# Kernel tuning notes

Hardware: AMD Instinct MI355X
Metric: run time of the kernel (lower is better)

Reference implementation:

```python
import jax, jax.numpy as jnp
import numpy as np

B, T, N, FI, FO = 4, 8, 1024, 64, 64
ALPHA = 0.2          # LeakyReLU negative slope
NEG_INF = -1e12      # matches torch's -1000000000000.0


def setup_inputs() -> dict:
    key = jax.random.key(0)
    k0, k1, k2, k3, k4 = jax.random.split(key, 5)
    inp = jax.random.normal(k0, (B, T, N, FI), dtype=jnp.float32)
    u = jax.random.uniform(k1, (T, N, N), dtype=jnp.float32)
    adj = jnp.where(u > 0.9, u, 0.0)
    # att_mask: [batch, node, seq] in {0,1}
    att_mask = (jax.random.uniform(k2, (B, N, T)) > 0.2).astype(jnp.float32)
    # xavier-ish init (gain 1.414)
    W = jax.random.normal(k3, (FI, FO), dtype=jnp.float32) * (1.414 * np.sqrt(2.0 / (FI + FO)))
    a = jax.random.normal(k4, (2 * FO, 1), dtype=jnp.float32) * (1.414 * np.sqrt(2.0 / (2 * FO + 1)))
    return {"adj": adj, "inp": inp, "att_mask": att_mask, "W": W, "a": a}


def reference(adj, inp, att_mask, W, a):
    Fo = W.shape[1]
    h = jnp.einsum('btnf,fo->btno', inp, W)               # [B,T,N,Fo]
    # additive decomposition of a^T [h_i || h_j] = a1.h_i + a2.h_j
    a1 = a[:Fo, 0]
    a2 = a[Fo:, 0]
    s1 = jnp.einsum('btno,o->btn', h, a1)                 # contributes along rows (i)
    s2 = jnp.einsum('btno,o->btn', h, a2)                 # contributes along cols (j)
    e = s1[..., :, None] + s2[..., None, :]               # [B,T,N,N]
    e = jnp.where(e > 0, e, ALPHA * e)                    # LeakyReLU
    att = jnp.where(adj > 0, e * adj, NEG_INF)            # adj broadcasts over batch
    att = jax.nn.softmax(att, axis=-1)
    m = jnp.transpose(att_mask, (0, 2, 1))                # [B,T,N]
    att = att * (m[..., :, None] * m[..., None, :])       # outer-product mask
    # dropout is identity in eval mode
    h_prime = jnp.einsum('btij,btjo->btio', att, h)       # [B,T,N,Fo]
    return jax.nn.elu(h_prime)                            # concat=True path
```

## Files before the change

### kernel.cpp

```cpp
#include <hip/hip_runtime.h>
#include <hip/hip_bf16.h>
#include <math.h>

#define N_NODES 1024
#define T_DIM 8

typedef __bf16 bf16x8 __attribute__((ext_vector_type(8)));
typedef float  f32x4  __attribute__((ext_vector_type(4)));

__device__ __forceinline__ float readlane_f(float v, int l) {
    return __uint_as_float(__builtin_amdgcn_readlane(__float_as_uint(v), l));
}

__global__ __launch_bounds__(256) void gat_h_kernel(
    const float* __restrict__ inp, const float* __restrict__ W,
    const float* __restrict__ a,
    __bf16* __restrict__ hT, float* __restrict__ s1w, float* __restrict__ s2w)
{
    __shared__ float Wl[64 * 64];
    __shared__ float xl[64 * 64];
    __shared__ __bf16 htl[64 * 66];

    const int tid  = threadIdx.x;
    const int blk  = blockIdx.x;
    const int bt   = blk >> 4;
    const int n0   = (blk & 15) * 64;
    const int lane = tid & 63;
    const int wave = tid >> 6;

    const float4* W4  = (const float4*)W;
    float4*       Wl4 = (float4*)Wl;
    const float4* x4  = (const float4*)(inp + (size_t)(bt * N_NODES + n0) * 64);
    float4*       xl4 = (float4*)xl;
#pragma unroll
    for (int k = 0; k < 4; ++k) {
        Wl4[tid + k * 256] = W4[tid + k * 256];
        xl4[tid + k * 256] = x4[tid + k * 256];
    }
    const float a1 = a[lane];
    const float a2 = a[64 + lane];
    __syncthreads();

#pragma unroll 1
    for (int rg = 0; rg < 16; rg += 4) {
        float xr[4], acc[4];
#pragma unroll
        for (int q = 0; q < 4; ++q) {
            xr[q]  = xl[(wave * 16 + rg + q) * 64 + lane];
            acc[q] = 0.f;
        }
#pragma unroll
        for (int f = 0; f < 64; ++f) {
            float w = Wl[f * 64 + lane];
#pragma unroll
            for (int q = 0; q < 4; ++q)
                acc[q] = fmaf(readlane_f(xr[q], f), w, acc[q]);
        }
#pragma unroll
        for (int q = 0; q < 4; ++q) {
            const int r = wave * 16 + rg + q;
            float v1 = acc[q] * a1, v2 = acc[q] * a2;
#pragma unroll
            for (int off = 32; off; off >>= 1) {
                v1 += __shfl_xor(v1, off, 64);
                v2 += __shfl_xor(v2, off, 64);
            }
            if (lane == 0) {
                s1w[bt * N_NODES + n0 + r] = v1;
                s2w[bt * N_NODES + n0 + r] = v2;
            }
            htl[lane * 66 + r] = (__bf16)acc[q];
        }
    }
    __syncthreads();

    {
        const int o  = tid >> 2;
        const int r0 = (tid & 3) * 16;
        unsigned u[8];
#pragma unroll
        for (int k = 0; k < 8; ++k)
            u[k] = *(const unsigned*)&htl[o * 66 + r0 + 2 * k];
        uint4* dst = (uint4*)(hT + (size_t)(bt * 64 + o) * N_NODES + n0 + r0);
        dst[0] = make_uint4(u[0], u[1], u[2], u[3]);
        dst[1] = make_uint4(u[4], u[5], u[6], u[7]);
    }
}

__global__ __launch_bounds__(64) void gat_attn_kernel(
    const float* __restrict__ adj, const float* __restrict__ att_mask,
    const __bf16* __restrict__ hT, const float* __restrict__ s1w,
    const float* __restrict__ s2w, float* __restrict__ out)
{
    __shared__ __align__(16) __bf16 p_l[16 * 72];

    const int bt    = blockIdx.y;
    const int b     = bt >> 3;
    const int t     = bt & 7;
    const int irow0 = blockIdx.x * 16;
    const int lane  = threadIdx.x;

    f32x4 acc[4];
#pragma unroll
    for (int nc = 0; nc < 4; ++nc) acc[nc] = (f32x4){0.f, 0.f, 0.f, 0.f};
    float lsum[16], s1v[16];
#pragma unroll
    for (int r = 0; r < 16; ++r) {
        lsum[r] = 0.f;
        s1v[r]  = s1w[bt * N_NODES + irow0 + r];
    }

    const float*  adjrow = adj + (size_t)t * N_NODES * N_NODES
                               + (size_t)irow0 * N_NODES + lane;
    const __bf16* hlane  = hT + (size_t)bt * 64 * N_NODES
                              + (size_t)(lane & 15) * N_NODES + (lane >> 4) * 8;
    const float*  s2bt   = s2w + bt * N_NODES;
    const float*  mbase  = att_mask + (size_t)b * N_NODES * T_DIM + t;
    __bf16* pwr = p_l + lane;
    const __bf16* prd = p_l + (lane & 15) * 72 + (lane >> 4) * 8;

    float  adjc[16];
    bf16x8 hc[8];
    float  s2c, mjc;
#pragma unroll
    for (int r = 0; r < 16; ++r) adjc[r] = adjrow[(size_t)r * N_NODES];
#pragma unroll
    for (int kc = 0; kc < 2; ++kc)
#pragma unroll
        for (int nc = 0; nc < 4; ++nc)
            hc[kc * 4 + nc] = *(const bf16x8*)(hlane + (size_t)nc * 16 * N_NODES + kc * 32);
    s2c = s2bt[lane];
    mjc = mbase[(size_t)lane * T_DIM];

#pragma unroll 2
    for (int it = 0; it < 16; ++it) {
        const int jn = (it < 15) ? (it + 1) * 64 : 0;

        float  adjn[16];
        bf16x8 hn[8];
#pragma unroll
        for (int r = 0; r < 16; ++r) adjn[r] = adjrow[(size_t)r * N_NODES + jn];
#pragma unroll
        for (int kc = 0; kc < 2; ++kc)
#pragma unroll
            for (int nc = 0; nc < 4; ++nc)
                hn[kc * 4 + nc] = *(const bf16x8*)(hlane + (size_t)nc * 16 * N_NODES + jn + kc * 32);
        const float s2n = s2bt[jn + lane];
        const float mjn = mbase[(size_t)(jn + lane) * T_DIM];

#pragma unroll
        for (int r = 0; r < 16; ++r) {
            float e = s1v[r] + s2c;
            e = (e > 0.f) ? e : 0.2f * e;
            float p = (adjc[r] > 0.f) ? __expf(e * adjc[r]) : 0.f;
            lsum[r] += p;
            pwr[r * 72] = (__bf16)(p * mjc);
        }

        bf16x8 af0 = *(const bf16x8*)(prd);
        bf16x8 af1 = *(const bf16x8*)(prd + 32);
#pragma unroll
        for (int nc = 0; nc < 4; ++nc)
            acc[nc] = __builtin_amdgcn_mfma_f32_16x16x32_bf16(af0, hc[nc], acc[nc], 0, 0, 0);
#pragma unroll
        for (int nc = 0; nc < 4; ++nc)
            acc[nc] = __builtin_amdgcn_mfma_f32_16x16x32_bf16(af1, hc[4 + nc], acc[nc], 0, 0, 0);

#pragma unroll
        for (int r = 0; r < 16; ++r) adjc[r] = adjn[r];
#pragma unroll
        for (int k = 0; k < 8; ++k) hc[k] = hn[k];
        s2c = s2n;
        mjc = mjn;
    }

#pragma unroll
    for (int r = 0; r < 16; ++r) {
#pragma unroll
        for (int off = 32; off; off >>= 1)
            lsum[r] += __shfl_xor(lsum[r], off, 64);
    }
    const int q = lane >> 4;
#pragma unroll
    for (int reg = 0; reg < 4; ++reg) {
        float ls = (q == 0) ? lsum[reg] : (q == 1) ? lsum[4 + reg]
                 : (q == 2) ? lsum[8 + reg] : lsum[12 + reg];
        const int i = irow0 + q * 4 + reg;
        float mi    = att_mask[((size_t)b * N_NODES + i) * T_DIM + t];
        float scale = mi / ls;
#pragma unroll
        for (int nc = 0; nc < 4; ++nc) {
            float v = acc[nc][reg] * scale;
            v = (v > 0.f) ? v : (__expf(v) - 1.f);
            out[((size_t)bt * N_NODES + i) * 64 + nc * 16 + (lane & 15)] = v;
        }
    }
}

extern "C" void kernel_launch(void* const* d_in, const int* in_sizes, int n_in,
                              void* d_out, int out_size, void* d_ws, size_t ws_size,
                              hipStream_t stream) {
    (void)in_sizes; (void)n_in; (void)out_size; (void)ws_size;
    const float* adj      = (const float*)d_in[0];
    const float* inp      = (const float*)d_in[1];
    const float* att_mask = (const float*)d_in[2];
    const float* W        = (const float*)d_in[3];
    const float* a        = (const float*)d_in[4];
    float* out = (float*)d_out;

    __bf16* hT  = (__bf16*)d_ws;
    float*  s1w = (float*)((char*)d_ws + (size_t)4 * 1024 * 1024);
    float*  s2w = s1w + 32 * N_NODES;

    gat_h_kernel<<<512, 256, 0, stream>>>(inp, W, a, hT, s1w, s2w);
    dim3 grid(64, 32);
    gat_attn_kernel<<<grid, 64, 0, stream>>>(adj, att_mask, hT, s1w, s2w, out);
}
```

Before: 140.6 us.

## Split attention key dimension across four waves with LDS reduction

The attention kernel now runs 256 threads per block, and each of four waves handles a quarter of the 1024 columns (j) for the same 16 rows. Each wave's partial MFMA accumulators and softmax row sums are written to shared memory and summed after a barrier before normalisation and ELU. The aim is more parallelism and latency hiding: 4x more waves over the same 2048 blocks, each with a shorter serial loop. The cost is extra LDS traffic, a block-wide sync, and a higher per-block LDS footprint.

Result: slower. 147.4 us (+4.8%).

```diff
diff --git a/kernel.cpp b/kernel.cpp
--- a/kernel.cpp
+++ b/kernel.cpp
@@ -87,18 +87,23 @@
     }
 }
 
-__global__ __launch_bounds__(64) void gat_attn_kernel(
+__global__ __launch_bounds__(256) void gat_attn_kernel(
     const float* __restrict__ adj, const float* __restrict__ att_mask,
     const __bf16* __restrict__ hT, const float* __restrict__ s1w,
     const float* __restrict__ s2w, float* __restrict__ out)
 {
-    __shared__ __align__(16) __bf16 p_l[16 * 72];
+    __shared__ __align__(16) __bf16 p_l[4][16 * 72];
+    __shared__ float accbuf[4][16][68];
+    __shared__ float lsumbuf[4][16];
 
     const int bt    = blockIdx.y;
     const int b     = bt >> 3;
     const int t     = bt & 7;
     const int irow0 = blockIdx.x * 16;
-    const int lane  = threadIdx.x;
+    const int tid   = threadIdx.x;
+    const int lane  = tid & 63;
+    const int wave  = tid >> 6;
+    const int j0    = wave * 256;
 
     f32x4 acc[4];
 #pragma unroll
@@ -111,13 +116,14 @@
     }
 
     const float*  adjrow = adj + (size_t)t * N_NODES * N_NODES
-                               + (size_t)irow0 * N_NODES + lane;
+                               + (size_t)irow0 * N_NODES + j0 + lane;
     const __bf16* hlane  = hT + (size_t)bt * 64 * N_NODES
-                              + (size_t)(lane & 15) * N_NODES + (lane >> 4) * 8;
-    const float*  s2bt   = s2w + bt * N_NODES;
-    const float*  mbase  = att_mask + (size_t)b * N_NODES * T_DIM + t;
-    __bf16* pwr = p_l + lane;
-    const __bf16* prd = p_l + (lane & 15) * 72 + (lane >> 4) * 8;
+                              + (size_t)(lane & 15) * N_NODES + j0 + (lane >> 4) * 8;
+    const float*  s2p    = s2w + bt * N_NODES + j0;
+    const float*  mp     = att_mask + (size_t)b * N_NODES * T_DIM + t
+                              + (size_t)j0 * T_DIM;
+    __bf16* pwr = p_l[wave] + lane;
+    const __bf16* prd = p_l[wave] + (lane & 15) * 72 + (lane >> 4) * 8;
 
     float  adjc[16];
     bf16x8 hc[8];
@@ -129,12 +135,12 @@
 #pragma unroll
         for (int nc = 0; nc < 4; ++nc)
             hc[kc * 4 + nc] = *(const bf16x8*)(hlane + (size_t)nc * 16 * N_NODES + kc * 32);
-    s2c = s2bt[lane];
-    mjc = mbase[(size_t)lane * T_DIM];
+    s2c = s2p[lane];
+    mjc = mp[(size_t)lane * T_DIM];
 
 #pragma unroll 2
-    for (int it = 0; it < 16; ++it) {
-        const int jn = (it < 15) ? (it + 1) * 64 : 0;
+    for (int it = 0; it < 4; ++it) {
+        const int jn = (it < 3) ? (it + 1) * 64 : 0;
 
         float  adjn[16];
         bf16x8 hn[8];
@@ -145,8 +151,8 @@
 #pragma unroll
             for (int nc = 0; nc < 4; ++nc)
                 hn[kc * 4 + nc] = *(const bf16x8*)(hlane + (size_t)nc * 16 * N_NODES + jn + kc * 32);
-        const float s2n = s2bt[jn + lane];
-        const float mjn = mbase[(size_t)(jn + lane) * T_DIM];
+        const float s2n = s2p[jn + lane];
+        const float mjn = mp[(size_t)(jn + lane) * T_DIM];
 
 #pragma unroll
         for (int r = 0; r < 16; ++r) {
@@ -180,19 +186,32 @@
         for (int off = 32; off; off >>= 1)
             lsum[r] += __shfl_xor(lsum[r], off, 64);
     }
-    const int q = lane >> 4;
-#pragma unroll
-    for (int reg = 0; reg < 4; ++reg) {
-        float ls = (q == 0) ? lsum[reg] : (q == 1) ? lsum[4 + reg]
-                 : (q == 2) ? lsum[8 + reg] : lsum[12 + reg];
-        const int i = irow0 + q * 4 + reg;
-        float mi    = att_mask[((size_t)b * N_NODES + i) * T_DIM + t];
+    if (lane == 0) {
+#pragma unroll
+        for (int r = 0; r < 16; ++r) lsumbuf[wave][r] = lsum[r];
+    }
+#pragma unroll
+    for (int nc = 0; nc < 4; ++nc)
+#pragma unroll
+        for (int reg = 0; reg < 4; ++reg)
+            accbuf[wave][(lane >> 4) * 4 + reg][nc * 16 + (lane & 15)] = acc[nc][reg];
+    __syncthreads();
+
+    {
+        const int row = tid >> 4;
+        const int c0  = tid & 15;
+        const int i   = irow0 + row;
+        float ls = lsumbuf[0][row] + lsumbuf[1][row]
+                 + lsumbuf[2][row] + lsumbuf[3][row];
+        float mi = att_mask[((size_t)b * N_NODES + i) * T_DIM + t];
         float scale = mi / ls;
 #pragma unroll
-        for (int nc = 0; nc < 4; ++nc) {
-            float v = acc[nc][reg] * scale;
+        for (int c = 0; c < 4; ++c) {
+            const int col = c * 16 + c0;
+            float v = (accbuf[0][row][col] + accbuf[1][row][col]
+                     + accbuf[2][row][col] + accbuf[3][row][col]) * scale;
             v = (v > 0.f) ? v : (__expf(v) - 1.f);
-            out[((size_t)bt * N_NODES + i) * 64 + nc * 16 + (lane & 15)] = v;
+            out[((size_t)bt * N_NODES + i) * 64 + col] = v;
         }
     }
 }
@@ -214,5 +233,5 @@
 
     gat_h_kernel<<<512, 256, 0, stream>>>(inp, W, a, hT, s1w, s2w);
     dim3 grid(64, 32);
-    gat_attn_kernel<<<grid, 64, 0, stream>>>(adj, att_mask, hT, s1w, s2w, out);
-}
+    gat_attn_kernel<<<grid, 256, 0, stream>>>(adj, att_mask, hT, s1w, s2w, out);
+}
```

## Fold column mask into h and prefetch adjacency two tiles ahead

Applied to the files above, without the earlier changes.

The column mask m_j is now multiplied into the bf16 h^T values in the projection kernel. This removes the strided att_mask gather and the per-element multiply from the attention inner loop. The adjacency tile loads are pipelined two iterations ahead instead of one, and the main loop is fully unrolled, to hide more HBM latency. The cost is extra registers (32 adjacency floats plus the h prefetch), which may lower occupancy, and the mask is now rounded to bf16 together with h.

Measured after the change: 146.0 us. +3.8%, slower.

```diff
diff --git a/kernel.cpp b/kernel.cpp
--- a/kernel.cpp
+++ b/kernel.cpp
@@ -14,7 +14,7 @@
 
 __global__ __launch_bounds__(256) void gat_h_kernel(
     const float* __restrict__ inp, const float* __restrict__ W,
-    const float* __restrict__ a,
+    const float* __restrict__ a, const float* __restrict__ att_mask,
     __bf16* __restrict__ hT, float* __restrict__ s1w, float* __restrict__ s2w)
 {
     __shared__ float Wl[64 * 64];
@@ -24,6 +24,8 @@
     const int tid  = threadIdx.x;
     const int blk  = blockIdx.x;
     const int bt   = blk >> 4;
+    const int b    = bt >> 3;
+    const int t    = bt & 7;
     const int n0   = (blk & 15) * 64;
     const int lane = tid & 63;
     const int wave = tid >> 6;
@@ -69,7 +71,8 @@
                 s1w[bt * N_NODES + n0 + r] = v1;
                 s2w[bt * N_NODES + n0 + r] = v2;
             }
-            htl[lane * 66 + r] = (__bf16)acc[q];
+            const float mjr = att_mask[((size_t)b * N_NODES + n0 + r) * T_DIM + t];
+            htl[lane * 66 + r] = (__bf16)(acc[q] * mjr);
         }
     }
     __syncthreads();
@@ -115,46 +118,46 @@
     const __bf16* hlane  = hT + (size_t)bt * 64 * N_NODES
                               + (size_t)(lane & 15) * N_NODES + (lane >> 4) * 8;
     const float*  s2bt   = s2w + bt * N_NODES;
-    const float*  mbase  = att_mask + (size_t)b * N_NODES * T_DIM + t;
     __bf16* pwr = p_l + lane;
     const __bf16* prd = p_l + (lane & 15) * 72 + (lane >> 4) * 8;
 
-    float  adjc[16];
+    float  adj0[16], adj1[16];
     bf16x8 hc[8];
-    float  s2c, mjc;
-#pragma unroll
-    for (int r = 0; r < 16; ++r) adjc[r] = adjrow[(size_t)r * N_NODES];
+    float  s2c;
+#pragma unroll
+    for (int r = 0; r < 16; ++r) {
+        adj0[r] = adjrow[(size_t)r * N_NODES];
+        adj1[r] = adjrow[(size_t)r * N_NODES + 64];
+    }
 #pragma unroll
     for (int kc = 0; kc < 2; ++kc)
 #pragma unroll
         for (int nc = 0; nc < 4; ++nc)
             hc[kc * 4 + nc] = *(const bf16x8*)(hlane + (size_t)nc * 16 * N_NODES + kc * 32);
     s2c = s2bt[lane];
-    mjc = mbase[(size_t)lane * T_DIM];
-
-#pragma unroll 2
+
+#pragma unroll
     for (int it = 0; it < 16; ++it) {
-        const int jn = (it < 15) ? (it + 1) * 64 : 0;
-
+        const int j2 = (it < 14) ? (it + 2) * 64 : 0;
+        const int j1 = (it < 15) ? (it + 1) * 64 : 0;
         float  adjn[16];
         bf16x8 hn[8];
 #pragma unroll
-        for (int r = 0; r < 16; ++r) adjn[r] = adjrow[(size_t)r * N_NODES + jn];
+        for (int r = 0; r < 16; ++r) adjn[r] = adjrow[(size_t)r * N_NODES + j2];
 #pragma unroll
         for (int kc = 0; kc < 2; ++kc)
 #pragma unroll
             for (int nc = 0; nc < 4; ++nc)
-                hn[kc * 4 + nc] = *(const bf16x8*)(hlane + (size_t)nc * 16 * N_NODES + jn + kc * 32);
-        const float s2n = s2bt[jn + lane];
-        const float mjn = mbase[(size_t)(jn + lane) * T_DIM];
+                hn[kc * 4 + nc] = *(const bf16x8*)(hlane + (size_t)nc * 16 * N_NODES + j1 + kc * 32);
+        const float s2n = s2bt[j1 + lane];
 
 #pragma unroll
         for (int r = 0; r < 16; ++r) {
             float e = s1v[r] + s2c;
             e = (e > 0.f) ? e : 0.2f * e;
-            float p = (adjc[r] > 0.f) ? __expf(e * adjc[r]) : 0.f;
+            float p = (adj0[r] > 0.f) ? __expf(e * adj0[r]) : 0.f;
             lsum[r] += p;
-            pwr[r * 72] = (__bf16)(p * mjc);
+            pwr[r * 72] = (__bf16)p;
         }
 
         bf16x8 af0 = *(const bf16x8*)(prd);
@@ -167,11 +170,10 @@
             acc[nc] = __builtin_amdgcn_mfma_f32_16x16x32_bf16(af1, hc[4 + nc], acc[nc], 0, 0, 0);
 
 #pragma unroll
-        for (int r = 0; r < 16; ++r) adjc[r] = adjn[r];
+        for (int r = 0; r < 16; ++r) { adj0[r] = adj1[r]; adj1[r] = adjn[r]; }
 #pragma unroll
         for (int k = 0; k < 8; ++k) hc[k] = hn[k];
         s2c = s2n;
-        mjc = mjn;
     }
 
 #pragma unroll
@@ -212,7 +214,7 @@
     float*  s1w = (float*)((char*)d_ws + (size_t)4 * 1024 * 1024);
     float*  s2w = s1w + 32 * N_NODES;
 
-    gat_h_kernel<<<512, 256, 0, stream>>>(inp, W, a, hT, s1w, s2w);
+    gat_h_kernel<<<512, 256, 0, stream>>>(inp, W, a, att_mask, hT, s1w, s2w);
     dim3 grid(64, 32);
     gat_attn_kernel<<<grid, 64, 0, stream>>>(adj, att_mask, hT, s1w, s2w, out);
 }
```
